# Optimization experiments

Measured on AMD Instinct MI355X. Metric: run time of the kernel, lower is better.

## Reference

```python
import jax, jax.numpy as jnp
import numpy as np

N, M, D = 16384, 1024, 32


def setup_inputs() -> dict:
    key = jax.random.key(0)
    k1, k2 = jax.random.split(key)
    x = jax.random.normal(k1, (N, D), dtype=jnp.float32)
    centers = jax.random.normal(k2, (M, D), dtype=jnp.float32)
    sigma = jnp.ones((M, D), dtype=jnp.float32)  # get_sigma_ones(s=1.0)
    return {"x": x, "centers": centers, "sigma": sigma}


def reference(x, centers, sigma):
    # Gaussian RBF kernel: exp(-0.5 * delta^T invCov delta) / sqrt((2pi)^D det(S))
    d = x.shape[1]
    s2 = sigma ** 2  # (M, D)
    # invCovMat: inverse of per-center diagonal covariance -> diag(1/s2)
    invCov = jnp.eye(d, dtype=x.dtype) * (1.0 / s2)[:, :, None]  # (M, D, D)
    # denom: sqrt((2pi)^D * prod(s2))
    k = (2.0 * np.pi) ** d  # python float, safe for D=32 in f32
    detS = jnp.sqrt(jnp.asarray(k, x.dtype) * jnp.prod(s2, axis=1))  # (M,)
    delta = x[:, None, :] - centers[None, :, :]  # (N, M, D)
    # batched (1,D) @ (D,D) per (n,m) pair, then elementwise * delta and reduce
    q = jnp.einsum('nmd,mde->nme', delta, invCov)  # (N, M, D)
    X = jnp.sum(q * delta, axis=2)  # (N, M) squared Mahalanobis distance
    return jnp.exp(-0.5 * X) / detS[None, :]  # (N, M)
```

## Files before the change

kernel.cpp:

```cpp
#include <hip/hip_runtime.h>


#define N_  16384
#define M_  1024
#define D_  32
#define NT  64
#define BLK 256

typedef float v2f __attribute__((ext_vector_type(2)));

__global__ __launch_bounds__(BLK) void rbf_kernel(
    const float* __restrict__ x, const float* __restrict__ centers,
    const float* __restrict__ sigma, float* __restrict__ out)
{
    const int tid = threadIdx.x;
    const int m   = blockIdx.x * BLK + tid;
    const int n0  = blockIdx.y * NT;

    __shared__ float r2s[NT];

    if (tid < NT) {
        const float4* xr = (const float4*)(x + (size_t)(n0 + tid) * D_);
        float a0 = 0.f, a1 = 0.f, a2 = 0.f, a3 = 0.f;
        #pragma unroll
        for (int k = 0; k < D_ / 4; ++k) {
            float4 v = xr[k];
            a0 = fmaf(v.x, v.x, a0); a1 = fmaf(v.y, v.y, a1);
            a2 = fmaf(v.z, v.z, a2); a3 = fmaf(v.w, v.w, a3);
        }
        r2s[tid] = (a0 + a1) + (a2 + a3);
    }
    __syncthreads();

    const float L2E      = 1.4426950408889634f;
    const float LOG2_2PI = 2.6514961294723187f;

    float s2_0 = 0.f, ld = 0.f;
    bool uf = true;
    {
        const float* sg = sigma + (size_t)m * D_;
        #pragma unroll
        for (int d = 0; d < D_; ++d) {
            float s  = sg[d];
            float s2 = s * s;
            if (d == 0) s2_0 = s2;
            uf = uf && (s2 == s2_0);
            ld += log2f(s2);
        }
    }

    if (__all((int)uf)) {
        const float w0 = 1.0f / s2_0;
        v2f av[D_ / 2];
        float b = 0.f;
        {
            const v2f* cg = (const v2f*)(centers + (size_t)m * D_);
            #pragma unroll
            for (int j = 0; j < D_ / 2; ++j) {
                v2f c = cg[j];
                v2f a = c * w0;
                av[j] = a;
                b = fmaf(c.x, a.x, b);
                b = fmaf(c.y, a.y, b);
            }
        }
        const float c0 = fmaf(-0.5f * L2E, b, -0.5f * (D_ * LOG2_2PI + ld));
        const float q  = -0.5f * L2E * w0;

        for (int i = 0; i < NT; ++i) {
            const v2f* xr = (const v2f*)(x + (size_t)(n0 + i) * D_);
            v2f acc0 = {0.f, 0.f}, acc1 = {0.f, 0.f};
            v2f acc2 = {0.f, 0.f}, acc3 = {0.f, 0.f};
            #pragma unroll
            for (int j = 0; j < D_ / 2; j += 4) {
                acc0 += xr[j + 0] * av[j + 0];
                acc1 += xr[j + 1] * av[j + 1];
                acc2 += xr[j + 2] * av[j + 2];
                acc3 += xr[j + 3] * av[j + 3];
            }
            v2f s = (acc0 + acc1) + (acc2 + acc3);
            float S2 = s.x + s.y;
            float f  = fmaf(L2E, S2, fmaf(q, r2s[i], c0));
            out[(size_t)(n0 + i) * M_ + m] = __builtin_amdgcn_exp2f(f);
        }
    } else {
        float wv[D_], cv[D_];
        {
            const float* sg = sigma   + (size_t)m * D_;
            const float* cg = centers + (size_t)m * D_;
            #pragma unroll
            for (int d = 0; d < D_; ++d) {
                float s = sg[d];
                wv[d] = 1.0f / (s * s);
                cv[d] = cg[d];
            }
        }
        const float c0 = -0.5f * (D_ * LOG2_2PI + ld);
        for (int i = 0; i < NT; ++i) {
            const float* xr = x + (size_t)(n0 + i) * D_;
            float a0 = 0.f, a1 = 0.f;
            #pragma unroll
            for (int d = 0; d < D_; d += 2) {
                float t0 = xr[d]     - cv[d];
                float t1 = xr[d + 1] - cv[d + 1];
                a0 = fmaf(t0 * wv[d],     t0, a0);
                a1 = fmaf(t1 * wv[d + 1], t1, a1);
            }
            float X = a0 + a1;
            float f = fmaf(-0.5f * L2E, X, c0);
            out[(size_t)(n0 + i) * M_ + m] = __builtin_amdgcn_exp2f(f);
        }
    }
}

extern "C" void kernel_launch(void* const* d_in, const int* in_sizes, int n_in,
                              void* d_out, int out_size, void* d_ws, size_t ws_size,
                              hipStream_t stream) {
    const float* x = (const float*)d_in[0];
    const float* c = (const float*)d_in[1];
    const float* s = (const float*)d_in[2];
    float* out = (float*)d_out;
    dim3 grid(M_ / BLK, N_ / NT);
    rbf_kernel<<<grid, BLK, 0, stream>>>(x, c, s, out);
}
```

Baseline: 96.05 us.

## Halve rows per block, process two rows per iteration, use nontemporal stores

Halves the rows per block so there are twice as many blocks for occupancy. The fast path now computes two x rows per loop iteration with rolled outer loop, and writes output with nontemporal stores to avoid cache pollution on the 64MB output stream. The fallback path drops per-thread register arrays in favour of reloading sigma/centers from memory each row, cutting register pressure at the cost of repeated loads. Each block now recomputes sigma log-det for fewer rows, adding redundant setup work.

```diff
diff --git a/kernel.cpp b/kernel.cpp
--- a/kernel.cpp
+++ b/kernel.cpp
@@ -4,7 +4,7 @@
 #define N_  16384
 #define M_  1024
 #define D_  32
-#define NT  64
+#define NT  32
 #define BLK 256
 
 typedef float v2f __attribute__((ext_vector_type(2)));
@@ -65,49 +65,46 @@
             }
         }
         const float c0 = fmaf(-0.5f * L2E, b, -0.5f * (D_ * LOG2_2PI + ld));
-        const float q  = -0.5f * L2E * w0;
+        const float qc = -0.5f * L2E * w0;
 
-        for (int i = 0; i < NT; ++i) {
-            const v2f* xr = (const v2f*)(x + (size_t)(n0 + i) * D_);
-            v2f acc0 = {0.f, 0.f}, acc1 = {0.f, 0.f};
-            v2f acc2 = {0.f, 0.f}, acc3 = {0.f, 0.f};
+        float* o0 = out + (size_t)n0 * M_ + m;
+        #pragma unroll 1
+        for (int i = 0; i < NT; i += 2) {
+            const v2f* xr0 = (const v2f*)(x + (size_t)(n0 + i) * D_);
+            const v2f* xr1 = xr0 + (D_ / 2);
+            v2f p0 = {0.f,0.f}, p1 = {0.f,0.f};
+            v2f q0 = {0.f,0.f}, q1 = {0.f,0.f};
             #pragma unroll
-            for (int j = 0; j < D_ / 2; j += 4) {
-                acc0 += xr[j + 0] * av[j + 0];
-                acc1 += xr[j + 1] * av[j + 1];
-                acc2 += xr[j + 2] * av[j + 2];
-                acc3 += xr[j + 3] * av[j + 3];
+            for (int j = 0; j < D_ / 2; j += 2) {
+                p0 += xr0[j]     * av[j];
+                p1 += xr0[j + 1] * av[j + 1];
+                q0 += xr1[j]     * av[j];
+                q1 += xr1[j + 1] * av[j + 1];
             }
-            v2f s = (acc0 + acc1) + (acc2 + acc3);
-            float S2 = s.x + s.y;
-            float f  = fmaf(L2E, S2, fmaf(q, r2s[i], c0));
-            out[(size_t)(n0 + i) * M_ + m] = __builtin_amdgcn_exp2f(f);
+            v2f ps = p0 + p1;
+            v2f qs = q0 + q1;
+            float f0 = fmaf(L2E, ps.x + ps.y, fmaf(qc, r2s[i],     c0));
+            float f1 = fmaf(L2E, qs.x + qs.y, fmaf(qc, r2s[i + 1], c0));
+            __builtin_nontemporal_store(__builtin_amdgcn_exp2f(f0), o0 + (size_t)i * M_);
+            __builtin_nontemporal_store(__builtin_amdgcn_exp2f(f1), o0 + (size_t)(i + 1) * M_);
         }
     } else {
-        float wv[D_], cv[D_];
-        {
-            const float* sg = sigma   + (size_t)m * D_;
-            const float* cg = centers + (size_t)m * D_;
-            #pragma unroll
-            for (int d = 0; d < D_; ++d) {
-                float s = sg[d];
-                wv[d] = 1.0f / (s * s);
-                cv[d] = cg[d];
-            }
-        }
         const float c0 = -0.5f * (D_ * LOG2_2PI + ld);
+        const float* cg = centers + (size_t)m * D_;
+        const float* sg = sigma   + (size_t)m * D_;
+        #pragma unroll 1
         for (int i = 0; i < NT; ++i) {
             const float* xr = x + (size_t)(n0 + i) * D_;
             float a0 = 0.f, a1 = 0.f;
             #pragma unroll
             for (int d = 0; d < D_; d += 2) {
-                float t0 = xr[d]     - cv[d];
-                float t1 = xr[d + 1] - cv[d + 1];
-                a0 = fmaf(t0 * wv[d],     t0, a0);
-                a1 = fmaf(t1 * wv[d + 1], t1, a1);
+                float s0 = sg[d], s1 = sg[d + 1];
+                float t0 = xr[d]     - cg[d];
+                float t1 = xr[d + 1] - cg[d + 1];
+                a0 = fmaf(t0 * (1.0f / (s0 * s0)), t0, a0);
+                a1 = fmaf(t1 * (1.0f / (s1 * s1)), t1, a1);
             }
-            float X = a0 + a1;
-            float f = fmaf(-0.5f * L2E, X, c0);
+            float f = fmaf(-0.5f * L2E, a0 + a1, c0);
             out[(size_t)(n0 + i) * M_ + m] = __builtin_amdgcn_exp2f(f);
         }
     }
```

After: 97.66 us. No clear change (+1.7%).
